# Kernel optimization log

Hardware: AMD Instinct MI355X
Metric: run time of the kernel (lower is better)

The kernel has to match this reference:

```python
import jax, jax.numpy as jnp
import numpy as np

TEMPERATURE = 0.02


def setup_inputs() -> dict:
    key = jax.random.key(0)
    kq, kp = jax.random.split(key)
    query_embeddings = jax.random.normal(kq, (32, 32, 128), dtype=jnp.float32)      # [b, s, h]
    positive_embeddings = jax.random.normal(kp, (512, 128, 128), dtype=jnp.float32)  # [c, d, h]
    return {"query_embeddings": query_embeddings, "positive_embeddings": positive_embeddings}


def reference(query_embeddings, positive_embeddings):
    # Late interaction: all query tokens vs all doc tokens across the (in-)batch.
    # [b, c, s, d]
    late = jnp.einsum('bsh,cdh->bcsd', query_embeddings, positive_embeddings)
    # MaxSim: max over doc tokens, sum over query tokens -> [b, c]
    scores = late.max(axis=-1).sum(axis=-1) / TEMPERATURE
    # CrossEntropyLoss(reduction='mean') with labels = zeros(b)
    loss = jnp.mean(jax.nn.logsumexp(scores, axis=-1) - scores[:, 0])
    return loss
```

## Files before the change

kernel.cpp:

```cpp
#include <hip/hip_runtime.h>

#define BQ 32
#define H  128
#define C  512
#define D  128

typedef _Float16 half8v __attribute__((ext_vector_type(8)));
typedef float floatx4 __attribute__((ext_vector_type(4)));

__global__ __launch_bounds__(256) void qprep_kernel(const float* __restrict__ q,
                                                    _Float16* __restrict__ qs,
                                                    float* __restrict__ out) {
  int t = blockIdx.x * 256 + threadIdx.x;
  if (t == 0) out[0] = 0.0f;
  int lane = t & 63;
  int sh   = (t >> 6) & 1;
  int kb   = (t >> 7) & 3;
  int b    = t >> 9;
  int s    = sh * 16 + (lane & 15);
  int h    = kb * 32 + (lane >> 4) * 8;
  const float* src = q + ((b * 32 + s) * H + h);
  float4 v0 = *(const float4*)src;
  float4 v1 = *(const float4*)(src + 4);
  half8v o = { (_Float16)v0.x, (_Float16)v0.y, (_Float16)v0.z, (_Float16)v0.w,
               (_Float16)v1.x, (_Float16)v1.y, (_Float16)v1.z, (_Float16)v1.w };
  *(half8v*)(qs + (size_t)t * 8) = o;
}

__global__ __launch_bounds__(256, 2) void scores_kernel(const float* __restrict__ pos,
                                                        const _Float16* __restrict__ qs,
                                                        float* __restrict__ scores) {
  const int c    = blockIdx.x;
  const int tid  = threadIdx.x;
  const int w    = tid >> 6;
  const int lane = tid & 63;
  const int dq   = w & 1;
  const int sh   = w >> 1;
  const int quad = lane >> 4;
  const int nrow = lane & 15;

  __shared__ float pmm[BQ][4][16];

  const half8v* qf = (const half8v*)qs;
  const float*  pc = pos + (size_t)c * (D * H);

  half8v  pa[4][4];
  half8v  qb[3][4];
  floatx4 acc[2][4];
  floatx4 zc = {0.f, 0.f, 0.f, 0.f};

#pragma unroll
  for (int kb = 0; kb < 4; ++kb)
#pragma unroll
    for (int mt = 0; mt < 4; ++mt) {
      const float* src = pc + ((dq * 64 + mt * 16 + nrow) * H + kb * 32 + quad * 8);
      float4 v0 = *(const float4*)src;
      float4 v1 = *(const float4*)(src + 4);
      half8v f = { (_Float16)v0.x, (_Float16)v0.y, (_Float16)v0.z, (_Float16)v0.w,
                   (_Float16)v1.x, (_Float16)v1.y, (_Float16)v1.z, (_Float16)v1.w };
      pa[mt][kb] = f;
    }

#pragma unroll
  for (int kb = 0; kb < 4; ++kb) qb[0][kb] = qf[(kb * 2 + sh) * 64 + lane];
#pragma unroll
  for (int kb = 0; kb < 4; ++kb) qb[1][kb] = qf[((4 + kb) * 2 + sh) * 64 + lane];

  auto reduce_store = [&](int b, floatx4 (&a)[4]) {
    float m0 = fmaxf(fmaxf(a[0][0], a[0][1]), fmaxf(a[0][2], a[0][3]));
    float m1 = fmaxf(fmaxf(a[1][0], a[1][1]), fmaxf(a[1][2], a[1][3]));
    float m2 = fmaxf(fmaxf(a[2][0], a[2][1]), fmaxf(a[2][2], a[2][3]));
    float m3 = fmaxf(fmaxf(a[3][0], a[3][1]), fmaxf(a[3][2], a[3][3]));
    float m  = fmaxf(fmaxf(m0, m1), fmaxf(m2, m3));
    m = fmaxf(m, __shfl_xor(m, 16));
    m = fmaxf(m, __shfl_xor(m, 32));
    if (lane < 16) pmm[b][w][lane] = m;
  };

#pragma unroll
  for (int mt = 0; mt < 4; ++mt)
    acc[0][mt] = __builtin_amdgcn_mfma_f32_16x16x32_f16(pa[mt][0], qb[0][0], zc, 0, 0, 0);
#pragma unroll
  for (int kb = 1; kb < 4; ++kb)
#pragma unroll
    for (int mt = 0; mt < 4; ++mt)
      acc[0][mt] = __builtin_amdgcn_mfma_f32_16x16x32_f16(pa[mt][kb], qb[0][kb], acc[0][mt], 0, 0, 0);

#pragma unroll
  for (int b = 1; b < BQ; ++b) {
    const int cur = b & 1, prv = cur ^ 1;
    if (b + 1 < BQ) {
      half8v* dst = qb[(b + 1) % 3];
#pragma unroll
      for (int kb = 0; kb < 4; ++kb) dst[kb] = qf[(((b + 1) * 4 + kb) * 2 + sh) * 64 + lane];
    }
    const half8v* qc = qb[b % 3];
#pragma unroll
    for (int mt = 0; mt < 4; ++mt)
      acc[cur][mt] = __builtin_amdgcn_mfma_f32_16x16x32_f16(pa[mt][0], qc[0], zc, 0, 0, 0);
#pragma unroll
    for (int kb = 1; kb < 4; ++kb)
#pragma unroll
      for (int mt = 0; mt < 4; ++mt)
        acc[cur][mt] = __builtin_amdgcn_mfma_f32_16x16x32_f16(pa[mt][kb], qc[kb], acc[cur][mt], 0, 0, 0);
    reduce_store(b - 1, acc[prv]);
  }
  reduce_store(BQ - 1, acc[1]);

  __syncthreads();

  {
    int b  = tid >> 3;
    int t8 = tid & 7;
    float v = 0.f;
#pragma unroll
    for (int j = 0; j < 4; ++j) {
      int s  = t8 * 4 + j;
      int h2 = s >> 4, sl = s & 15;
      v += fmaxf(pmm[b][2 * h2][sl], pmm[b][2 * h2 + 1][sl]);
    }
    v += __shfl_xor(v, 1);
    v += __shfl_xor(v, 2);
    v += __shfl_xor(v, 4);
    if (t8 == 0) scores[b * C + c] = v * 50.0f;
  }
}

__global__ __launch_bounds__(256) void loss_kernel(const float* __restrict__ scores,
                                                   float* __restrict__ out) {
  __shared__ float red[8];
  const int b = blockIdx.x, tid = threadIdx.x, w = tid >> 6, lane = tid & 63;
  const float* row = scores + b * C;
  float x0 = row[tid], x1 = row[tid + 256];
  float mx = fmaxf(x0, x1);
#pragma unroll
  for (int off = 1; off < 64; off <<= 1) mx = fmaxf(mx, __shfl_xor(mx, off));
  if (lane == 0) red[w] = mx;
  __syncthreads();
  float bmax = fmaxf(fmaxf(red[0], red[1]), fmaxf(red[2], red[3]));
  float e = __expf(x0 - bmax) + __expf(x1 - bmax);
#pragma unroll
  for (int off = 1; off < 64; off <<= 1) e += __shfl_xor(e, off);
  if (lane == 0) red[4 + w] = e;
  __syncthreads();
  if (tid == 0) {
    float s = red[4] + red[5] + red[6] + red[7];
    atomicAdd(out, (bmax + __logf(s) - row[0]) * (1.0f / 32.0f));
  }
}

extern "C" void kernel_launch(void* const* d_in, const int* in_sizes, int n_in,
                              void* d_out, int out_size, void* d_ws, size_t ws_size,
                              hipStream_t stream) {
  const float* q = (const float*)d_in[0];
  const float* p = (const float*)d_in[1];
  float* scores  = (float*)d_ws;
  _Float16* qs   = (_Float16*)((char*)d_ws + 65536);

  qprep_kernel<<<64, 256, 0, stream>>>(q, qs, (float*)d_out);
  scores_kernel<<<C, 256, 0, stream>>>(p, qs, scores);
  loss_kernel<<<32, 256, 0, stream>>>(scores, (float*)d_out);
}
```

Baseline: 94.26 us.

## Split each doc block across two query halves and raise occupancy hint

The scores kernel now launches two blocks per document, each handling 16 of the 32 query batches, with the grid doubled and the launch bound raised to three blocks per CU. This exposes more parallelism on a 256-CU device where 512 blocks gave only about two waves of work, improving load balance and latency hiding. The cost is that each document's fp32 embeddings are loaded and converted to fp16 twice, doubling the dominant global read traffic, and the tighter register budget may cause spills.

```diff
diff --git a/kernel.cpp b/kernel.cpp
--- a/kernel.cpp
+++ b/kernel.cpp
@@ -27,10 +27,11 @@
   *(half8v*)(qs + (size_t)t * 8) = o;
 }
 
-__global__ __launch_bounds__(256, 2) void scores_kernel(const float* __restrict__ pos,
+__global__ __launch_bounds__(256, 3) void scores_kernel(const float* __restrict__ pos,
                                                         const _Float16* __restrict__ qs,
                                                         float* __restrict__ scores) {
-  const int c    = blockIdx.x;
+  const int c    = blockIdx.x >> 1;
+  const int bh   = blockIdx.x & 1;
   const int tid  = threadIdx.x;
   const int w    = tid >> 6;
   const int lane = tid & 63;
@@ -39,10 +40,11 @@
   const int quad = lane >> 4;
   const int nrow = lane & 15;
 
-  __shared__ float pmm[BQ][4][16];
+  __shared__ float pmm[16][4][16];
 
   const half8v* qf = (const half8v*)qs;
   const float*  pc = pos + (size_t)c * (D * H);
+  const int     b0 = bh * 16;
 
   half8v  pa[4][4];
   half8v  qb[3][4];
@@ -62,11 +64,11 @@
     }
 
 #pragma unroll
-  for (int kb = 0; kb < 4; ++kb) qb[0][kb] = qf[(kb * 2 + sh) * 64 + lane];
+  for (int kb = 0; kb < 4; ++kb) qb[0][kb] = qf[((b0 * 4 + kb) * 2 + sh) * 64 + lane];
 #pragma unroll
-  for (int kb = 0; kb < 4; ++kb) qb[1][kb] = qf[((4 + kb) * 2 + sh) * 64 + lane];
+  for (int kb = 0; kb < 4; ++kb) qb[1][kb] = qf[(((b0 + 1) * 4 + kb) * 2 + sh) * 64 + lane];
 
-  auto reduce_store = [&](int b, floatx4 (&a)[4]) {
+  auto reduce_store = [&](int lb, floatx4 (&a)[4]) {
     float m0 = fmaxf(fmaxf(a[0][0], a[0][1]), fmaxf(a[0][2], a[0][3]));
     float m1 = fmaxf(fmaxf(a[1][0], a[1][1]), fmaxf(a[1][2], a[1][3]));
     float m2 = fmaxf(fmaxf(a[2][0], a[2][1]), fmaxf(a[2][2], a[2][3]));
@@ -74,27 +76,19 @@
     float m  = fmaxf(fmaxf(m0, m1), fmaxf(m2, m3));
     m = fmaxf(m, __shfl_xor(m, 16));
     m = fmaxf(m, __shfl_xor(m, 32));
-    if (lane < 16) pmm[b][w][lane] = m;
+    if (lane < 16) pmm[lb][w][lane] = m;
   };
 
 #pragma unroll
-  for (int mt = 0; mt < 4; ++mt)
-    acc[0][mt] = __builtin_amdgcn_mfma_f32_16x16x32_f16(pa[mt][0], qb[0][0], zc, 0, 0, 0);
+  for (int lb = 0; lb < 16; ++lb) {
+    const int cur = lb & 1;
+    if (lb + 2 < 16) {
+      const int gb = b0 + lb + 2;
+      half8v* dst = qb[(lb + 2) % 3];
 #pragma unroll
-  for (int kb = 1; kb < 4; ++kb)
-#pragma unroll
-    for (int mt = 0; mt < 4; ++mt)
-      acc[0][mt] = __builtin_amdgcn_mfma_f32_16x16x32_f16(pa[mt][kb], qb[0][kb], acc[0][mt], 0, 0, 0);
-
-#pragma unroll
-  for (int b = 1; b < BQ; ++b) {
-    const int cur = b & 1, prv = cur ^ 1;
-    if (b + 1 < BQ) {
-      half8v* dst = qb[(b + 1) % 3];
-#pragma unroll
-      for (int kb = 0; kb < 4; ++kb) dst[kb] = qf[(((b + 1) * 4 + kb) * 2 + sh) * 64 + lane];
+      for (int kb = 0; kb < 4; ++kb) dst[kb] = qf[((gb * 4 + kb) * 2 + sh) * 64 + lane];
     }
-    const half8v* qc = qb[b % 3];
+    const half8v* qc = qb[lb % 3];
 #pragma unroll
     for (int mt = 0; mt < 4; ++mt)
       acc[cur][mt] = __builtin_amdgcn_mfma_f32_16x16x32_f16(pa[mt][0], qc[0], zc, 0, 0, 0);
@@ -103,26 +97,26 @@
 #pragma unroll
       for (int mt = 0; mt < 4; ++mt)
         acc[cur][mt] = __builtin_amdgcn_mfma_f32_16x16x32_f16(pa[mt][kb], qc[kb], acc[cur][mt], 0, 0, 0);
-    reduce_store(b - 1, acc[prv]);
+    if (lb > 0) reduce_store(lb - 1, acc[cur ^ 1]);
   }
-  reduce_store(BQ - 1, acc[1]);
+  reduce_store(15, acc[1]);
 
   __syncthreads();
 
-  {
-    int b  = tid >> 3;
+  if (tid < 128) {
+    int lb = tid >> 3;
     int t8 = tid & 7;
     float v = 0.f;
 #pragma unroll
     for (int j = 0; j < 4; ++j) {
       int s  = t8 * 4 + j;
       int h2 = s >> 4, sl = s & 15;
-      v += fmaxf(pmm[b][2 * h2][sl], pmm[b][2 * h2 + 1][sl]);
+      v += fmaxf(pmm[lb][2 * h2][sl], pmm[lb][2 * h2 + 1][sl]);
     }
     v += __shfl_xor(v, 1);
     v += __shfl_xor(v, 2);
     v += __shfl_xor(v, 4);
-    if (t8 == 0) scores[b * C + c] = v * 50.0f;
+    if (t8 == 0) scores[(b0 + lb) * C + c] = v * 50.0f;
   }
 }
 
@@ -158,6 +152,6 @@
   _Float16* qs   = (_Float16*)((char*)d_ws + 65536);
 
   qprep_kernel<<<64, 256, 0, stream>>>(q, qs, (float*)d_out);
-  scores_kernel<<<C, 256, 0, stream>>>(p, qs, scores);
+  scores_kernel<<<2 * C, 256, 0, stream>>>(p, qs, scores);
   loss_kernel<<<32, 256, 0, stream>>>(scores, (float*)d_out);
 }
```

Measured after the change: 99.51 us. 5.6% more time.
